# Performance work log

Hardware: AMD Instinct MI355X
Metric: run time of the kernel (lower is better)

## Reference

```python
import jax, jax.numpy as jnp
import numpy as np

T, B, C, HF, H, W, E, TOP_K = 4, 32, 384, 1536, 14, 14, 8, 2
AUX_W = 0.01
ALPHA = 2.0  # spikingjelly ATan surrogate default

@jax.custom_vjp
def spike(v):
    return (v >= 0.0).astype(v.dtype)

def _spike_fwd(v):
    return spike(v), v

def _spike_bwd(v, g):
    sg = (ALPHA / 2.0) / (1.0 + (jnp.pi / 2.0 * ALPHA * v) ** 2)
    return (g * sg,)

spike.defvjp(_spike_fwd, _spike_bwd)

def lif_multistep(x, tau):
    # x: (T, ...). decay_input=True, v_threshold=1, hard reset to 0, detach_reset
    def step(v, xt):
        v = v + (xt - v) / tau
        s = spike(v - 1.0)
        v = v * (1.0 - jax.lax.stop_gradient(s))
        return v, s
    _, s = jax.lax.scan(step, jnp.zeros_like(x[0]), x)
    return s

def bn_eval(y, gamma, beta, mean, var, eps=1e-5):
    inv = gamma / jnp.sqrt(var + eps)
    return y * inv[None, :, None, None] + (beta - mean * inv)[None, :, None, None]

def setup_inputs() -> dict:
    key = jax.random.key(0)
    ks = jax.random.split(key, 8)
    d = {"x": jax.random.normal(ks[0], (T, B, C, H, W), jnp.float32)}
    d["rw"] = jax.random.normal(ks[1], (E, C), jnp.float32) * 0.02
    d["rb"] = jnp.zeros((E,), jnp.float32)
    d["r_gamma"] = jnp.ones((E,), jnp.float32)
    d["r_beta"] = jnp.zeros((E,), jnp.float32)
    d["r_mean"] = jax.random.normal(ks[2], (E,), jnp.float32) * 0.01
    d["r_var"] = jax.random.uniform(ks[3], (E,), jnp.float32, 0.75, 1.25)
    d["w1"] = jax.random.normal(ks[4], (E, HF, C), jnp.float32) * 0.02
    d["b1"] = jnp.zeros((E, HF), jnp.float32)
    d["g1"] = jnp.ones((E, HF), jnp.float32)
    d["be1"] = jnp.zeros((E, HF), jnp.float32)
    d["m1"] = jax.random.normal(ks[5], (E, HF), jnp.float32) * 0.01
    d["v1"] = jnp.ones((E, HF), jnp.float32)
    d["w2"] = jax.random.normal(ks[6], (E, C, HF), jnp.float32) * 0.02
    d["b2"] = jnp.zeros((E, C), jnp.float32)
    d["g2"] = jnp.ones((E, C), jnp.float32)
    d["be2"] = jnp.zeros((E, C), jnp.float32)
    d["m2"] = jax.random.normal(ks[7], (E, C), jnp.float32) * 0.01
    d["v2"] = jnp.ones((E, C), jnp.float32)
    d["taus"] = jnp.linspace(1.5, 4.0, E, dtype=jnp.float32)
    return d

def reference(x, rw, rb, r_gamma, r_beta, r_mean, r_var,
              w1, b1, g1, be1, m1, v1, w2, b2, g2, be2, m2, v2, taus):
    Tn, Bn, Cn, Hn, Wn = x.shape
    N = Tn * Bn
    # ---- SpikeRouter ----
    s = lif_multistep(x, 2.0)                                   # (T,B,C,H,W)
    r = jnp.einsum('tbchw,ec->tbehw', s, rw) + rb[None, None, :, None, None]
    r = bn_eval(r.reshape(N, E, Hn, Wn), r_gamma, r_beta, r_mean, r_var)
    logits = r.mean(axis=(-2, -1))                              # (N,E)
    probs = jax.nn.softmax(logits, axis=-1)
    tkw, tki = jax.lax.top_k(probs, TOP_K)
    tkw = tkw / tkw.sum(axis=-1, keepdims=True)
    one_hot = jax.nn.one_hot(tki, E, dtype=x.dtype)             # (N,K,E)
    gate = (one_hot * tkw[..., None]).sum(axis=1)               # (N,E), 0 for unselected
    # ---- expert dispatch/combine (dense, math-equivalent: gate==0 masks out) ----
    xt = x.reshape(N, Cn, Hn, Wn)
    out = jnp.zeros_like(xt)
    for e in range(E):
        s1 = spike(xt / taus[e] - 1.0)                          # T=1 LIF step
        h = jnp.einsum('nchw,oc->nohw', s1, w1[e]) + b1[e][None, :, None, None]
        h = bn_eval(h, g1[e], be1[e], m1[e], v1[e])
        s2 = spike(h / taus[e] - 1.0)
        o = jnp.einsum('nchw,oc->nohw', s2, w2[e]) + b2[e][None, :, None, None]
        o = bn_eval(o, g2[e], be2[e], m2[e], v2[e])
        o = o + xt                                              # final residual
        out = out + gate[:, e, None, None, None] * o
    # ---- Switch-style load balancing loss ----
    f = one_hot.sum(axis=1).mean(axis=0)                        # fraction routed per expert
    p = probs.mean(axis=0)
    aux = AUX_W * E * jnp.sum(f * p)
    return out.reshape(Tn, Bn, Cn, Hn, Wn), aux
```

## Files before the change

kernel.cpp:

```cpp
#include <hip/hip_runtime.h>
#include <hip/hip_bf16.h>
#include <cstdint>
#include <math.h>

#define T_  4
#define B_  32
#define C_  384
#define HF_ 1536
#define HW_ 196
#define E_  8
#define N_  128
#define NROW 1792
#define NGT  50176
#define LCAP 64

#define LIFB (B_ * C_)
#define TRB  (E_ * 12 * 24)
#define PRB  48

__global__ __launch_bounds__(256) void k_lifprep(
    const float* __restrict__ x, float* __restrict__ cnt,
    const float* __restrict__ w1, __hip_bfloat16* __restrict__ w1t,
    const float* b1, const float* g1, const float* be1,
    const float* m1, const float* v1,
    const float* b2, const float* g2, const float* be2,
    const float* m2, const float* v2,
    const float* taus,
    float* A, float* Bc, float* const2, float* inv2v,
    float* rowmaxp, int* header) {
  __shared__ float tile[64][33];
  __shared__ int c4[T_];
  int blk = blockIdx.x;
  int tid = threadIdx.x;

  if (blk < LIFB) {
    if (tid < T_) c4[tid] = 0;
    __syncthreads();
    int bc = blk;
    bool act = tid < HW_;
    float v = 0.f;
    size_t base = (size_t)bc * HW_ + (act ? tid : 0);
    #pragma unroll
    for (int t = 0; t < T_; ++t) {
      float xv = act ? x[base + (size_t)t * B_ * C_ * HW_] : -1e30f;
      v = v + (xv - v) * 0.5f;
      bool sp = (v - 1.0f >= 0.0f);
      if (sp) v = 0.f;
      unsigned long long m = __ballot(act && sp);
      if ((tid & 63) == 0) atomicAdd(&c4[t], __popcll(m));
    }
    __syncthreads();
    if (tid < T_) cnt[(size_t)tid * B_ * C_ + bc] = (float)c4[tid];
  } else if (blk < LIFB + TRB) {
    int rem = blk - LIFB;
    int e = rem / 288, r2 = rem % 288;
    int ct = r2 / 24, ot = r2 % 24;
    int c0 = ct * 32, o0 = ot * 64;
    int cl = tid & 31, olb = tid >> 5;
    #pragma unroll
    for (int it = 0; it < 8; ++it) {
      int ol = olb + it * 8;
      tile[ol][cl] = w1[(size_t)(e * HF_ + o0 + ol) * C_ + c0 + cl];
    }
    __syncthreads();
    int ol2 = tid & 63, clb = tid >> 6;
    #pragma unroll
    for (int it = 0; it < 8; ++it) {
      int cl2 = clb + it * 4;
      w1t[(size_t)(e * C_ + c0 + cl2) * HF_ + o0 + ol2] =
          __float2bfloat16(tile[ol2][cl2]);
    }
    if (tid < 32) {
      float m = 0.f;
      for (int ol = 0; ol < 64; ++ol) {
        float bv = __bfloat162float(__float2bfloat16(tile[ol][tid]));
        m = fmaxf(m, fabsf(bv));
      }
      rowmaxp[(size_t)(e * C_ + c0 + tid) * 24 + ot] = m;
    }
  } else {
    int idx = (blk - LIFB - TRB) * 256 + tid;
    if (idx < 64) header[idx] = 0;
    if (idx < E_ * HF_) {
      int e = idx / HF_;
      float inv = g1[idx] / sqrtf(v1[idx] + 1e-5f);
      float sh  = be1[idx] - m1[idx] * inv;
      A[idx]  = inv;
      Bc[idx] = inv * b1[idx] + sh - taus[e];
    }
    if (idx < E_ * C_) {
      float inv = g2[idx] / sqrtf(v2[idx] + 1e-5f);
      const2[idx] = b2[idx] * inv + (be2[idx] - m2[idx] * inv);
      inv2v[idx]  = inv;
    }
  }
}

__global__ __launch_bounds__(256) void k_router(
    const float* __restrict__ cnt, const float* __restrict__ rw,
    const float* rb, const float* rg, const float* rbeta,
    const float* rmean, const float* rvar,
    const float* __restrict__ const2,
    const float* __restrict__ rowmaxp, float* __restrict__ rowmax,
    const float* __restrict__ A, const float* __restrict__ Bc,
    float* __restrict__ thrmin,
    int* sel_e, float* sel_g, float* gsum, float* K,
    float* f_acc, float* p_acc) {
  __shared__ float sc[C_ + 256 + E_];
  __shared__ int s_i1, s_i2;
  __shared__ float s_g1, s_g2;
  int bid = blockIdx.x, tid = threadIdx.x;

  if (bid < N_) {
    int n = bid;
    float* part = sc + C_;
    float* lg = part + 256;
    for (int c = tid; c < C_; c += 256) sc[c] = cnt[(size_t)n * C_ + c];
    __syncthreads();
    {
      int e = tid >> 5, sub = tid & 31;
      float d = 0.f;
      for (int c = sub; c < C_; c += 32) d += rw[e * C_ + c] * sc[c];
      part[tid] = d;
    }
    __syncthreads();
    if (tid < E_) {
      float dot = 0.f;
      #pragma unroll
      for (int j = 0; j < 32; ++j) dot += part[tid * 32 + j];
      float inv = rg[tid] / sqrtf(rvar[tid] + 1e-5f);
      lg[tid] = (dot * (1.0f / HW_) + rb[tid]) * inv +
                (rbeta[tid] - rmean[tid] * inv);
    }
    __syncthreads();
    if (tid == 0) {
      float m = lg[0];
      for (int e = 1; e < E_; ++e) m = fmaxf(m, lg[e]);
      float pr[E_]; float s = 0.f;
      for (int e = 0; e < E_; ++e) { pr[e] = expf(lg[e] - m); s += pr[e]; }
      float invs = 1.0f / s;
      for (int e = 0; e < E_; ++e) pr[e] *= invs;
      int i1 = 0;
      for (int e = 1; e < E_; ++e) if (pr[e] > pr[i1]) i1 = e;
      int i2 = (i1 == 0) ? 1 : 0;
      for (int e = 0; e < E_; ++e) if (e != i1 && pr[e] > pr[i2]) i2 = e;
      float w = pr[i1] + pr[i2];
      float ga = pr[i1] / w, gb = pr[i2] / w;
      sel_e[2 * n] = i1; sel_e[2 * n + 1] = i2;
      sel_g[2 * n] = ga; sel_g[2 * n + 1] = gb;
      gsum[n] = ga + gb;
      s_i1 = i1; s_i2 = i2; s_g1 = ga; s_g2 = gb;
      atomicAdd(&f_acc[i1], 1.0f);
      atomicAdd(&f_acc[i2], 1.0f);
      for (int e = 0; e < E_; ++e) atomicAdd(&p_acc[e], pr[e]);
    }
    __syncthreads();
    int i1 = s_i1, i2 = s_i2; float ga = s_g1, gb = s_g2;
    for (int c = tid; c < C_; c += 256)
      K[(size_t)n * C_ + c] =
          ga * const2[i1 * C_ + c] + gb * const2[i2 * C_ + c];
  } else if (bid < N_ + 12) {
    int idx = (bid - N_) * 256 + tid;
    if (idx < E_ * C_) {
      float m = 0.f;
      #pragma unroll
      for (int t = 0; t < 24; ++t) m = fmaxf(m, rowmaxp[(size_t)idx * 24 + t]);
      rowmax[idx] = m;
    }
  } else {
    float* red = sc;
    for (int e = 0; e < E_; ++e) {
      float m = INFINITY;
      for (int o = tid; o < HF_; o += 256) {
        float a = A[e * HF_ + o], b = Bc[e * HF_ + o];
        float thr = (a != 0.0f) ? (-b / fabsf(a))
                                : ((b >= 0.0f) ? -INFINITY : INFINITY);
        m = fminf(m, thr);
      }
      red[tid] = m;
      __syncthreads();
      for (int s = 128; s > 0; s >>= 1) {
        if (tid < s) red[tid] = fminf(red[tid], red[tid + s]);
        __syncthreads();
      }
      if (tid == 0) thrmin[e] = red[0];
      __syncthreads();
    }
  }
}

__global__ __launch_bounds__(256) void k_lists(
    const float* __restrict__ x, const int* __restrict__ sel_e,
    const float* __restrict__ taus, const float* __restrict__ rowmax,
    const float* __restrict__ thrmin,
    unsigned short* __restrict__ list16,
    int* __restrict__ queue, int* __restrict__ qcount,
    const float* __restrict__ f_acc, const float* __restrict__ p_acc,
    float* __restrict__ aux_out) {
  __shared__ float xs[14 * 385];
  int bid = blockIdx.x, tid = threadIdx.x;
  int lane = tid & 63, wave = tid >> 6;
  int n = bid / 14, h = bid - n * 14;
  unsigned long long lmask = (1ull << lane) - 1ull;

  if (bid == 0 && tid == 0) {
    float s = 0.f;
    for (int e = 0; e < E_; ++e)
      s += (f_acc[e] * (1.0f / N_)) * (p_acc[e] * (1.0f / N_));
    *aux_out = 0.01f * E_ * s;
  }

  for (int idx = tid; idx < C_ * 7; idx += 256) {
    int c = idx / 7, wp = idx - c * 7;
    float2 v = *(const float2*)(x + ((size_t)(n * C_ + c) * 14 + h) * 14 + 2 * wp);
    xs[(2 * wp) * 385 + c]     = v.x;
    xs[(2 * wp + 1) * 385 + c] = v.y;
  }
  __syncthreads();

  for (int t = wave; t < 28; t += 4) {
    int k = t / 14, w = t - k * 14;
    int pair = 2 * n + k;
    int e = sel_e[pair];
    float tau = taus[e];
    const float* rme = rowmax + e * C_;
    unsigned long long masks[6];
    int nnz = 0;
    float myb = 0.f;
    #pragma unroll
    for (int cb = 0; cb < 6; ++cb) {
      int c = cb * 64 + lane;
      bool sp = (xs[w * 385 + c] / tau - 1.0f >= 0.0f);
      unsigned long long m = __ballot(sp);
      masks[cb] = m;
      if (sp) myb += rme[c];
      nnz += __popcll(m);
    }
    #pragma unroll
    for (int off = 1; off < 64; off <<= 1) myb += __shfl_xor(myb, off, 64);
    bool prune = (myb < thrmin[e] - 1e-4f);
    if (!prune) {
      int tw = pair * 196 + h * 14 + w;
      size_t lbase = (size_t)tw * LCAP;
      int cum = 0;
      #pragma unroll
      for (int cb = 0; cb < 6; ++cb) {
        unsigned long long m = masks[cb];
        bool sp = (m >> lane) & 1ull;
        int pos = cum + __popcll(m & lmask);
        if (sp && pos < LCAP) list16[lbase + pos] = (unsigned short)(cb * 64 + lane);
        cum += __popcll(m);
      }
      if (lane == 0) {
        int nv = nnz < LCAP ? nnz : LCAP;
        int qi = atomicAdd(qcount, 1);
        queue[qi] = tw | (nv << 20);
      }
    }
  }
}

__global__ __launch_bounds__(256) void k_combine(
    const float* __restrict__ x, const float* __restrict__ gsum,
    const float* __restrict__ K, float* __restrict__ out) {
  int idx = blockIdx.x * 256 + threadIdx.x;
  int nc = idx / 49;
  float g = gsum[nc / C_];
  float kc = K[nc];
  float4 v = ((const float4*)x)[idx];
  v.x = g * v.x + kc;
  v.y = g * v.y + kc;
  v.z = g * v.z + kc;
  v.w = g * v.w + kc;
  ((float4*)out)[idx] = v;
}

__global__ __launch_bounds__(256, 4) void k_gather(
    const __hip_bfloat16* __restrict__ w1t,
    const float* __restrict__ A, const float* __restrict__ Bc,
    const int* __restrict__ sel_e, const float* __restrict__ sel_g,
    const int* __restrict__ queue, const int* __restrict__ qcount,
    const unsigned short* __restrict__ list16,
    const float* __restrict__ inv2v, const float* __restrict__ w2,
    float* __restrict__ out) {
  int nq = *qcount;
  int wid = blockIdx.x * 4 + (threadIdx.x >> 6);
  int lane = threadIdx.x & 63;
  int nwaves = gridDim.x * 4;

  for (int qi = wid; qi < nq; qi += nwaves) {
    int ent = queue[qi];
    int tw = ent & 0xFFFFF;
    int nnz = ent >> 20;
    int pair = tw / HW_, pos = tw - pair * HW_;
    int n = pair >> 1;
    int e = sel_e[pair];
    int lv = (int)list16[(size_t)tw * LCAP + lane];
    const uint4* wb = (const uint4*)(w1t + (size_t)e * C_ * HF_);

    #pragma unroll
    for (int pass = 0; pass < 3; ++pass) {
      const uint4* wbp = wb + pass * 64 + lane;
      float acc[8];
      #pragma unroll
      for (int q = 0; q < 8; ++q) acc[q] = 0.f;
      int j = 0;
      for (; j + 4 <= nnz; j += 4) {
        int c0 = __shfl(lv, j + 0);
        int c1 = __shfl(lv, j + 1);
        int c2 = __shfl(lv, j + 2);
        int c3 = __shfl(lv, j + 3);
        uint4 a = wbp[c0 * 192];
        uint4 b = wbp[c1 * 192];
        uint4 c = wbp[c2 * 192];
        uint4 d = wbp[c3 * 192];
        uint32_t ua[4] = {a.x, a.y, a.z, a.w};
        uint32_t ub[4] = {b.x, b.y, b.z, b.w};
        uint32_t uc[4] = {c.x, c.y, c.z, c.w};
        uint32_t ud[4] = {d.x, d.y, d.z, d.w};
        #pragma unroll
        for (int q = 0; q < 4; ++q) {
          acc[2 * q]     += __uint_as_float(ua[q] << 16) + __uint_as_float(ub[q] << 16) +
                            __uint_as_float(uc[q] << 16) + __uint_as_float(ud[q] << 16);
          acc[2 * q + 1] += __uint_as_float(ua[q] & 0xffff0000u) + __uint_as_float(ub[q] & 0xffff0000u) +
                            __uint_as_float(uc[q] & 0xffff0000u) + __uint_as_float(ud[q] & 0xffff0000u);
        }
      }
      for (; j < nnz; ++j) {
        int c0 = __shfl(lv, j);
        uint4 a = wbp[c0 * 192];
        uint32_t ua[4] = {a.x, a.y, a.z, a.w};
        #pragma unroll
        for (int q = 0; q < 4; ++q) {
          acc[2 * q]     += __uint_as_float(ua[q] << 16);
          acc[2 * q + 1] += __uint_as_float(ua[q] & 0xffff0000u);
        }
      }
      int k2 = (pass * 64 + lane) * 2;
      float4 Av0 = ((const float4*)(A + e * HF_))[k2];
      float4 Av1 = ((const float4*)(A + e * HF_))[k2 + 1];
      float4 Bv0 = ((const float4*)(Bc + e * HF_))[k2];
      float4 Bv1 = ((const float4*)(Bc + e * HF_))[k2 + 1];
      float av[8] = {Av0.x, Av0.y, Av0.z, Av0.w, Av1.x, Av1.y, Av1.z, Av1.w};
      float bv[8] = {Bv0.x, Bv0.y, Bv0.z, Bv0.w, Bv1.x, Bv1.y, Bv1.z, Bv1.w};
      #pragma unroll
      for (int q = 0; q < 8; ++q) {
        unsigned long long fm = __ballot(av[q] * acc[q] + bv[q] >= 0.0f);
        while (fm) {
          int b = __ffsll((unsigned long long)fm) - 1;
          fm &= fm - 1;
          int o = (pass * 64 + b) * 8 + q;
          float gk = sel_g[pair];
          const float* w2r = w2 + (size_t)e * C_ * HF_ + o;
          const float* ivr = inv2v + e * C_;
          for (int c = lane; c < C_; c += 64) {
            atomicAdd(&out[((size_t)(n * C_ + c)) * HW_ + pos],
                      gk * ivr[c] * w2r[(size_t)c * HF_]);
          }
        }
      }
    }
  }
}

extern "C" void kernel_launch(void* const* d_in, const int* in_sizes, int n_in,
                              void* d_out, int out_size, void* d_ws, size_t ws_size,
                              hipStream_t stream) {
  const float* x       = (const float*)d_in[0];
  const float* rw      = (const float*)d_in[1];
  const float* rb      = (const float*)d_in[2];
  const float* r_gamma = (const float*)d_in[3];
  const float* r_beta  = (const float*)d_in[4];
  const float* r_mean  = (const float*)d_in[5];
  const float* r_var   = (const float*)d_in[6];
  const float* w1      = (const float*)d_in[7];
  const float* b1      = (const float*)d_in[8];
  const float* g1      = (const float*)d_in[9];
  const float* be1     = (const float*)d_in[10];
  const float* m1      = (const float*)d_in[11];
  const float* v1      = (const float*)d_in[12];
  const float* w2      = (const float*)d_in[13];
  const float* b2      = (const float*)d_in[14];
  const float* g2      = (const float*)d_in[15];
  const float* be2     = (const float*)d_in[16];
  const float* m2      = (const float*)d_in[17];
  const float* v2      = (const float*)d_in[18];
  const float* taus    = (const float*)d_in[19];
  float* out = (float*)d_out;

  char* ws = (char*)d_ws;
  int*   header = (int*)ws;
  float* f_acc  = (float*)ws + 8;
  float* p_acc  = (float*)ws + 16;
  float* cnt    = (float*)(ws + 256);
  int*   sel_e  = (int*)(ws + 196864);
  float* sel_g  = (float*)(ws + 197888);
  float* gsum   = (float*)(ws + 198912);
  float* K      = (float*)(ws + 199424);
  float* A      = (float*)(ws + 396032);
  float* Bc     = (float*)(ws + 445184);
  float* const2 = (float*)(ws + 494336);
  float* inv2v  = (float*)(ws + 506624);
  __hip_bfloat16* w1t = (__hip_bfloat16*)(ws + 715520);
  int*   queue  = (int*)(ws + 10152704);
  unsigned short* list16 = (unsigned short*)(ws + 10353408);
  float* rowmaxp = (float*)(ws + 16775936);
  float* rowmax  = (float*)(ws + 17070848);
  float* thrmin  = (float*)(ws + 17083136);
  int* qcount = header + 1;

  k_lifprep<<<LIFB + TRB + PRB, 256, 0, stream>>>(
      x, cnt, w1, w1t, b1, g1, be1, m1, v1, b2, g2, be2, m2, v2, taus,
      A, Bc, const2, inv2v, rowmaxp, header);
  k_router<<<N_ + 13, 256, 0, stream>>>(
      cnt, rw, rb, r_gamma, r_beta, r_mean, r_var, const2,
      rowmaxp, rowmax, A, Bc, thrmin,
      sel_e, sel_g, gsum, K, f_acc, p_acc);
  k_lists<<<NROW, 256, 0, stream>>>(
      x, sel_e, taus, rowmax, thrmin, list16, queue, qcount,
      f_acc, p_acc, out + (out_size - 1));
  k_combine<<<(N_ * C_ * 49) / 256, 256, 0, stream>>>(x, gsum, K, out);
  k_gather<<<2048, 256, 0, stream>>>(
      w1t, A, Bc, sel_e, sel_g, queue, qcount, list16, inv2v, w2, out);
}
```

Measured before the change: 221.1 us.

## Vectorize LIF counting per wave, fuse combine into lists, precompute spike thresholds

The LIF spike-count stage now handles one (b,c) row per wavefront using float4 loads and packed per-timestep counters reduced with shuffles. This replaces one block per row with shared-memory atomics and cuts the block count by four. The combine kernel is folded into the k_lists launch as extra blocks, saving one launch and letting the two overlap. The per-element x/tau-1>=0 test is replaced by a comparison against a precomputed per-expert threshold, found by stepping down one ulp at a time to match the division-based rounding. That threshold search only checks four ulps, so exact equivalence to the original spike test is a risk.

```diff
diff --git a/kernel.cpp b/kernel.cpp
--- a/kernel.cpp
+++ b/kernel.cpp
@@ -14,9 +14,10 @@
 #define NGT  50176
 #define LCAP 64
 
-#define LIFB (B_ * C_)
+#define LIFW (B_ * C_ / 4)
 #define TRB  (E_ * 12 * 24)
 #define PRB  48
+#define COMBB ((N_ * C_ * 49) / 256)
 
 __global__ __launch_bounds__(256) void k_lifprep(
     const float* __restrict__ x, float* __restrict__ cnt,
@@ -27,32 +28,46 @@
     const float* m2, const float* v2,
     const float* taus,
     float* A, float* Bc, float* const2, float* inv2v,
-    float* rowmaxp, int* header) {
+    float* rowmaxp, int* header, float* te_g) {
   __shared__ float tile[64][33];
-  __shared__ int c4[T_];
   int blk = blockIdx.x;
   int tid = threadIdx.x;
 
-  if (blk < LIFB) {
-    if (tid < T_) c4[tid] = 0;
-    __syncthreads();
-    int bc = blk;
-    bool act = tid < HW_;
-    float v = 0.f;
-    size_t base = (size_t)bc * HW_ + (act ? tid : 0);
+  if (blk < LIFW) {
+    int lane = tid & 63, wave = tid >> 6;
+    int bc = blk * 4 + wave;
+    bool act = lane < 49;
+    const float4* xr = (const float4*)x;
+    size_t rb = (size_t)bc * 49 + (act ? lane : 0);
+    const size_t ts4 = (size_t)B_ * C_ * 49;
+    float4 v = {0.f, 0.f, 0.f, 0.f};
+    unsigned int counts = 0;
     #pragma unroll
     for (int t = 0; t < T_; ++t) {
-      float xv = act ? x[base + (size_t)t * B_ * C_ * HW_] : -1e30f;
-      v = v + (xv - v) * 0.5f;
-      bool sp = (v - 1.0f >= 0.0f);
-      if (sp) v = 0.f;
-      unsigned long long m = __ballot(act && sp);
-      if ((tid & 63) == 0) atomicAdd(&c4[t], __popcll(m));
-    }
-    __syncthreads();
-    if (tid < T_) cnt[(size_t)tid * B_ * C_ + bc] = (float)c4[tid];
-  } else if (blk < LIFB + TRB) {
-    int rem = blk - LIFB;
+      float4 xv;
+      if (act) xv = xr[rb + (size_t)t * ts4];
+      else { xv.x = xv.y = xv.z = xv.w = -1e30f; }
+      v.x = v.x + (xv.x - v.x) * 0.5f;
+      v.y = v.y + (xv.y - v.y) * 0.5f;
+      v.z = v.z + (xv.z - v.z) * 0.5f;
+      v.w = v.w + (xv.w - v.w) * 0.5f;
+      int cl = 0;
+      if (v.x - 1.0f >= 0.0f) { v.x = 0.f; ++cl; }
+      if (v.y - 1.0f >= 0.0f) { v.y = 0.f; ++cl; }
+      if (v.z - 1.0f >= 0.0f) { v.z = 0.f; ++cl; }
+      if (v.w - 1.0f >= 0.0f) { v.w = 0.f; ++cl; }
+      counts += (unsigned int)cl << (8 * t);
+    }
+    #pragma unroll
+    for (int off = 1; off < 64; off <<= 1)
+      counts += (unsigned int)__shfl_xor((int)counts, off, 64);
+    if (lane == 0) {
+      #pragma unroll
+      for (int t = 0; t < T_; ++t)
+        cnt[(size_t)t * B_ * C_ + bc] = (float)((counts >> (8 * t)) & 0xffu);
+    }
+  } else if (blk < LIFW + TRB) {
+    int rem = blk - LIFW;
     int e = rem / 288, r2 = rem % 288;
     int ct = r2 / 24, ot = r2 % 24;
     int c0 = ct * 32, o0 = ot * 64;
@@ -79,8 +94,18 @@
       rowmaxp[(size_t)(e * C_ + c0 + tid) * 24 + ot] = m;
     }
   } else {
-    int idx = (blk - LIFB - TRB) * 256 + tid;
+    int idx = (blk - LIFW - TRB) * 256 + tid;
     if (idx < 64) header[idx] = 0;
+    if (idx < E_) {
+      float t = taus[idx];
+      float y = t;
+      #pragma unroll
+      for (int it = 0; it < 4; ++it) {
+        float cnd = __uint_as_float(__float_as_uint(y) - 1u);
+        if (cnd / t - 1.0f >= 0.0f) y = cnd; else break;
+      }
+      te_g[idx] = y;
+    }
     if (idx < E_ * HF_) {
       int e = idx / HF_;
       float inv = g1[idx] / sqrtf(v1[idx] + 1e-5f);
@@ -191,14 +216,31 @@
 
 __global__ __launch_bounds__(256) void k_lists(
     const float* __restrict__ x, const int* __restrict__ sel_e,
-    const float* __restrict__ taus, const float* __restrict__ rowmax,
+    const float* __restrict__ te_g, const float* __restrict__ rowmax,
     const float* __restrict__ thrmin,
     unsigned short* __restrict__ list16,
     int* __restrict__ queue, int* __restrict__ qcount,
     const float* __restrict__ f_acc, const float* __restrict__ p_acc,
-    float* __restrict__ aux_out) {
+    float* __restrict__ aux_out,
+    const float* __restrict__ gsum, const float* __restrict__ K,
+    float* __restrict__ out) {
   __shared__ float xs[14 * 385];
   int bid = blockIdx.x, tid = threadIdx.x;
+
+  if (bid >= NROW) {
+    int idx = (bid - NROW) * 256 + tid;
+    int nc = idx / 49;
+    float g = gsum[nc / C_];
+    float kc = K[nc];
+    float4 v = ((const float4*)x)[idx];
+    v.x = g * v.x + kc;
+    v.y = g * v.y + kc;
+    v.z = g * v.z + kc;
+    v.w = g * v.w + kc;
+    ((float4*)out)[idx] = v;
+    return;
+  }
+
   int lane = tid & 63, wave = tid >> 6;
   int n = bid / 14, h = bid - n * 14;
   unsigned long long lmask = (1ull << lane) - 1ull;
@@ -222,7 +264,7 @@
     int k = t / 14, w = t - k * 14;
     int pair = 2 * n + k;
     int e = sel_e[pair];
-    float tau = taus[e];
+    float tee = te_g[e];
     const float* rme = rowmax + e * C_;
     unsigned long long masks[6];
     int nnz = 0;
@@ -230,7 +272,7 @@
     #pragma unroll
     for (int cb = 0; cb < 6; ++cb) {
       int c = cb * 64 + lane;
-      bool sp = (xs[w * 385 + c] / tau - 1.0f >= 0.0f);
+      bool sp = (xs[w * 385 + c] >= tee);
       unsigned long long m = __ballot(sp);
       masks[cb] = m;
       if (sp) myb += rme[c];
@@ -258,21 +300,6 @@
       }
     }
   }
-}
-
-__global__ __launch_bounds__(256) void k_combine(
-    const float* __restrict__ x, const float* __restrict__ gsum,
-    const float* __restrict__ K, float* __restrict__ out) {
-  int idx = blockIdx.x * 256 + threadIdx.x;
-  int nc = idx / 49;
-  float g = gsum[nc / C_];
-  float kc = K[nc];
-  float4 v = ((const float4*)x)[idx];
-  v.x = g * v.x + kc;
-  v.y = g * v.y + kc;
-  v.z = g * v.z + kc;
-  v.w = g * v.w + kc;
-  ((float4*)out)[idx] = v;
 }
 
 __global__ __launch_bounds__(256, 4) void k_gather(
@@ -407,19 +434,19 @@
   float* rowmaxp = (float*)(ws + 16775936);
   float* rowmax  = (float*)(ws + 17070848);
   float* thrmin  = (float*)(ws + 17083136);
+  float* te_g    = (float*)(ws + 17083200);
   int* qcount = header + 1;
 
-  k_lifprep<<<LIFB + TRB + PRB, 256, 0, stream>>>(
+  k_lifprep<<<LIFW + TRB + PRB, 256, 0, stream>>>(
       x, cnt, w1, w1t, b1, g1, be1, m1, v1, b2, g2, be2, m2, v2, taus,
-      A, Bc, const2, inv2v, rowmaxp, header);
+      A, Bc, const2, inv2v, rowmaxp, header, te_g);
   k_router<<<N_ + 13, 256, 0, stream>>>(
       cnt, rw, rb, r_gamma, r_beta, r_mean, r_var, const2,
       rowmaxp, rowmax, A, Bc, thrmin,
       sel_e, sel_g, gsum, K, f_acc, p_acc);
-  k_lists<<<NROW, 256, 0, stream>>>(
-      x, sel_e, taus, rowmax, thrmin, list16, queue, qcount,
-      f_acc, p_acc, out + (out_size - 1));
-  k_combine<<<(N_ * C_ * 49) / 256, 256, 0, stream>>>(x, gsum, K, out);
+  k_lists<<<NROW + COMBB, 256, 0, stream>>>(
+      x, sel_e, te_g, rowmax, thrmin, list16, queue, qcount,
+      f_acc, p_acc, out + (out_size - 1), gsum, K, out);
   k_gather<<<2048, 256, 0, stream>>>(
       w1t, A, Bc, sel_e, sel_g, queue, qcount, list16, inv2v, w2, out);
 }
```

Result: faster. 201.7 us (-8.8%).
